# Optimization experiments

Measured on AMD Instinct MI355X. Metric: run time of the kernel, lower is better.

Reference implementation:

```python
import jax, jax.numpy as jnp
import numpy as np

N = 100000      # nodes
E = 1600000     # edges (before self loops)
F_IN = 128      # num_features
HEADS1, CH1 = 8, 8    # conv1: heads=8, out=8, concat -> 64
HEADS2, CH2 = 1, 16   # conv2: heads=1, out=16, concat=False
B = 64          # graphs in batch


def setup_inputs() -> dict:
    key = jax.random.key(0)
    ks = jax.random.split(key, 20)
    s = 0.05
    x = jax.random.normal(ks[0], (N, F_IN), dtype=jnp.float32)
    edge_index = jax.random.randint(ks[1], (2, E), 0, N, dtype=jnp.int64)
    batch = jnp.sort(jax.random.randint(ks[2], (N,), 0, B, dtype=jnp.int64))
    d = {
        'x': x, 'edge_index': edge_index, 'batch': batch,
        # conv1 params (GATv2: lin_l / lin_r with bias, att vector, output bias)
        'Wl1': jax.random.normal(ks[3], (F_IN, HEADS1 * CH1)) * s,
        'bl1': jnp.zeros((HEADS1 * CH1,), jnp.float32),
        'Wr1': jax.random.normal(ks[4], (F_IN, HEADS1 * CH1)) * s,
        'br1': jnp.zeros((HEADS1 * CH1,), jnp.float32),
        'att1': jax.random.normal(ks[5], (HEADS1, CH1)) * s,
        'bias1': jnp.zeros((HEADS1 * CH1,), jnp.float32),
        # conv2 params
        'Wl2': jax.random.normal(ks[6], (HEADS1 * CH1, HEADS2 * CH2)) * s,
        'bl2': jnp.zeros((HEADS2 * CH2,), jnp.float32),
        'Wr2': jax.random.normal(ks[7], (HEADS1 * CH1, HEADS2 * CH2)) * s,
        'br2': jnp.zeros((HEADS2 * CH2,), jnp.float32),
        'att2': jax.random.normal(ks[8], (HEADS2, CH2)) * s,
        'bias2': jnp.zeros((CH2,), jnp.float32),
        # classifier 16 -> 1
        'Wc': jax.random.normal(ks[9], (CH2, 1)) * s,
        'bc': jnp.zeros((1,), jnp.float32),
    }
    return d


def gatv2_layer(x, src, dst, Wl, bl, Wr, br, att, bias, heads, ch, concat):
    n = x.shape[0]
    xl = (x @ Wl + bl).reshape(n, heads, ch)   # source transform (messages)
    xr = (x @ Wr + br).reshape(n, heads, ch)   # target transform
    m = xl[src] + xr[dst]                      # [E, H, C]
    e = jax.nn.leaky_relu(m, 0.2)
    logits = jnp.einsum('ehc,hc->eh', e, att)  # [E, H]
    # segment softmax over incoming edges per target node
    mx = jax.ops.segment_max(logits, dst, num_segments=n)
    mx = jnp.where(jnp.isfinite(mx), mx, 0.0)
    ex = jnp.exp(logits - mx[dst])
    denom = jax.ops.segment_sum(ex, dst, num_segments=n)
    alpha = ex / (denom[dst] + 1e-16)
    out = jax.ops.segment_sum(alpha[:, :, None] * xl[src], dst, num_segments=n)
    out = out.reshape(n, heads * ch) if concat else out.mean(axis=1)
    return out + bias


def reference(x, edge_index, batch, Wl1, bl1, Wr1, br1, att1, bias1,
              Wl2, bl2, Wr2, br2, att2, bias2, Wc, bc):
    n = x.shape[0]
    loops = jnp.arange(n, dtype=edge_index.dtype)
    src = jnp.concatenate([edge_index[0], loops])   # add self loops (PyG default)
    dst = jnp.concatenate([edge_index[1], loops])

    h = gatv2_layer(x, src, dst, Wl1, bl1, Wr1, br1, att1, bias1, HEADS1, CH1, True)
    h = jax.nn.elu(h)
    h = gatv2_layer(h, src, dst, Wl2, bl2, Wr2, br2, att2, bias2, HEADS2, CH2, False)

    counts = jax.ops.segment_sum(jnp.ones((n,), h.dtype), batch, num_segments=B)
    pooled = jax.ops.segment_sum(h, batch, num_segments=B) / jnp.clip(counts, 1.0)[:, None]
    out = (pooled @ Wc + bc).reshape(-1)            # [B]
    return out, pooled
```

## Files before the change

kernel.cpp:

```cpp
#include <hip/hip_runtime.h>
#include <cstdint>
#include <cstddef>

#define F_IN   128
#define HC1    64
#define CH2_   16
#define NB     64
#define BUKPAD 8192

__global__ void fill_f32(float* __restrict__ p, float v, int n) {
  int i = blockIdx.x * blockDim.x + threadIdx.x;
  int stride = gridDim.x * blockDim.x;
  for (; i < n; i += stride) p[i] = v;
}

__device__ __forceinline__ unsigned short f2bf_rne(float v) {
  unsigned int u = __float_as_uint(v);
  unsigned int r = (u + 0x7FFFu + ((u >> 16) & 1u)) >> 16;
  return (unsigned short)r;
}
__device__ __forceinline__ float bf2f(unsigned short b) {
  return __uint_as_float((unsigned int)b << 16);
}

template<int CTRL>
__device__ __forceinline__ float dpp_add(float v) {
  int j = __builtin_amdgcn_update_dpp(0, __float_as_int(v), CTRL, 0xF, 0xF, true);
  return v + __int_as_float(j);
}
__device__ __forceinline__ float sum16_dpp(float v) {
  v = dpp_add<0xB1>(v);
  v = dpp_add<0x4E>(v);
  v = dpp_add<0x141>(v);
  v = dpp_add<0x140>(v);
  return v;
}

__global__ void gemm_dual_l1(const float* __restrict__ x,
                             const float* __restrict__ Wa, const float* __restrict__ ba,
                             const float* __restrict__ Wb, const float* __restrict__ bb,
                             unsigned short* __restrict__ ya, float* __restrict__ yb, int n) {
  constexpr int K = F_IN, M = HC1, BM = 64, NN = 16;
  __shared__ float xs[BM * K];
  const int t = threadIdx.x;
  const int node0 = blockIdx.x * BM;
  for (int i = t; i < BM * (K / 4); i += 256) {
    int row = i / (K / 4);
    int kk  = (i % (K / 4)) * 4;
    int node = node0 + row;
    float4 v = make_float4(0.f, 0.f, 0.f, 0.f);
    if (node < n) v = *reinterpret_cast<const float4*>(x + (size_t)node * K + kk);
    *reinterpret_cast<float4*>(xs + row * K + kk) = v;
  }
  __syncthreads();
  const int col = t % M;
  const int ng  = t / M;
  float accA[NN], accB[NN];
  const float biasA = ba[col], biasB = bb[col];
#pragma unroll
  for (int i = 0; i < NN; ++i) { accA[i] = biasA; accB[i] = biasB; }
  for (int k = 0; k < K; k += 4) {
    float wa0 = Wa[(k + 0) * M + col], wa1 = Wa[(k + 1) * M + col];
    float wa2 = Wa[(k + 2) * M + col], wa3 = Wa[(k + 3) * M + col];
    float wb0 = Wb[(k + 0) * M + col], wb1 = Wb[(k + 1) * M + col];
    float wb2 = Wb[(k + 2) * M + col], wb3 = Wb[(k + 3) * M + col];
#pragma unroll
    for (int nn = 0; nn < NN; ++nn) {
      float4 xv = *reinterpret_cast<const float4*>(xs + (ng * NN + nn) * K + k);
      accA[nn] += xv.x * wa0 + xv.y * wa1 + xv.z * wa2 + xv.w * wa3;
      accB[nn] += xv.x * wb0 + xv.y * wb1 + xv.z * wb2 + xv.w * wb3;
    }
  }
#pragma unroll
  for (int nn = 0; nn < NN; ++nn) {
    int node = node0 + ng * NN + nn;
    if (node < n) {
      ya[(size_t)node * M + col] = f2bf_rne(accA[nn]);
      yb[(size_t)node * M + col] = accB[nn];
    }
  }
}


__global__ void bucket_scatter(const int* __restrict__ ei, int E, int E2,
                               int* __restrict__ gcnt, int* __restrict__ gbuk) {
  __shared__ int hbase[512];
  __shared__ int hcnt[512];
  const int t = threadIdx.x;
  for (int i = t; i < 512; i += 256) { hbase[i] = 0; hcnt[i] = 0; }
  __syncthreads();
  int srcs[32], dsts[32];
  const int tile0 = blockIdx.x * 8192;
#pragma unroll
  for (int k = 0; k < 32; ++k) {
    int e = tile0 + k * 256 + t;
    int s = -1, d = 0;
    if (e < E2) {
      if (e < E) { s = ei[e]; d = ei[E + e]; } else { s = d = e - E; }
      atomicAdd(&hbase[d >> 8], 1);
    }
    srcs[k] = s; dsts[k] = d;
  }
  __syncthreads();
  for (int i = t; i < 512; i += 256) {
    int c = hbase[i];
    hbase[i] = (c > 0) ? atomicAdd(&gcnt[i], c) : 0;
  }
  __syncthreads();
#pragma unroll
  for (int k = 0; k < 32; ++k) {
    if (srcs[k] >= 0) {
      int d = dsts[k], b = d >> 8;
      int r = atomicAdd(&hcnt[b], 1);
      int pl = hbase[b] + r;
      if (pl < BUKPAD) gbuk[(size_t)b * BUKPAD + pl] = (srcs[k] << 8) | (d & 255);
    }
  }
}

__global__ void bucket_prefix(const int* __restrict__ gcnt, int nbuk,
                              int* __restrict__ gbase, int* __restrict__ row_start, int n) {
  int lane = threadIdx.x;
  int carry = 0;
  for (int basei = 0; basei < nbuk; basei += 64) {
    int i = basei + lane;
    int orig = (i < nbuk) ? gcnt[i] : 0;
    int v = orig;
    for (int off = 1; off < 64; off <<= 1) {
      int u = __shfl_up(v, off);
      if (lane >= off) v += u;
    }
    if (i < nbuk) gbase[i] = carry + v - orig;
    carry += __shfl(v, 63);
  }
  if (lane == 0) row_start[n] = carry;
}

__global__ void bucket_csr(const int* __restrict__ gcnt, const int* __restrict__ gbase,
                           const int* __restrict__ gbuk,
                           int* __restrict__ row_start, int* __restrict__ csr_src, int n) {
  const int b = blockIdx.x;
  const int t = threadIdx.x;
  const int node0 = b << 8;
  const int cntb = min(gcnt[b], BUKPAD);
  const int base = gbase[b];
  const int* buk = gbuk + (size_t)b * BUKPAD;
  __shared__ int h[256];
  __shared__ int off[256];
  h[t] = 0;
  __syncthreads();
  for (int i = t; i < cntb; i += 256) atomicAdd(&h[buk[i] & 255], 1);
  __syncthreads();
  off[t] = h[t];
  __syncthreads();
  for (int o = 1; o < 256; o <<= 1) {
    int u = (t >= o) ? off[t - o] : 0;
    __syncthreads();
    off[t] += u;
    __syncthreads();
  }
  int excl = off[t] - h[t];
  if (node0 + t < n) row_start[node0 + t] = base + excl;
  h[t] = excl;
  __syncthreads();
  for (int i = t; i < cntb; i += 256) {
    int p = buk[i];
    int r = atomicAdd(&h[p & 255], 1);
    csr_src[base + r] = p >> 8;
  }
}

__global__ void fused_layer1(const int* __restrict__ row_start, const int* __restrict__ csr_src,
                             const unsigned short* __restrict__ xl, const float* __restrict__ xr,
                             const float* __restrict__ att, const float* __restrict__ bias,
                             const float* __restrict__ Wl2, const float* __restrict__ bl2,
                             const float* __restrict__ Wr2, const float* __restrict__ br2,
                             float* __restrict__ xl2, float* __restrict__ xr2, int n) {
  __shared__ float Ws2[64 * 32];
  __shared__ float b2s[32];
  const int t = threadIdx.x;
  for (int i = t; i < 64 * 16; i += 256) {
    int l = i >> 4, j = i & 15;
    Ws2[l * 32 + j]      = Wl2[i];
    Ws2[l * 32 + 16 + j] = Wr2[i];
  }
  if (t < 16) { b2s[t] = bl2[t]; b2s[16 + t] = br2[t]; }
  __syncthreads();

  const int node = blockIdx.x * 4 + (t >> 6);
  if (node >= n) return;
  const int lane = t & 63;
  const int g = lane >> 4;
  const int q = lane & 15;
  const float4 attv = *reinterpret_cast<const float4*>(att + q * 4);
  const float4 xrv  = *reinterpret_cast<const float4*>(xr + (size_t)node * 64 + q * 4);
  const unsigned short* xlq = xl + q * 4;
  const int beg = row_start[node];
  const int total = row_start[node + 1] - beg;
  const float NEGB = -3.0e38f;
  float den = 0.0f;
  float4 acc = make_float4(0.f, 0.f, 0.f, 0.f);

  for (int base = 0; base < total; base += 64) {
    int idx = base + lane;
    int sidx = csr_src[beg + (idx < total ? idx : total - 1)];
    const int lim = min(64, total - base);
    for (int c0 = 0; c0 < lim; c0 += 8) {
      int iA = c0 + g, iB = c0 + 4 + g;
      int sA = __shfl(sidx, iA);
      int sB = __shfl(sidx, iB);
      ushort4 uA = *reinterpret_cast<const ushort4*>(xlq + (size_t)sA * 64);
      ushort4 uB = *reinterpret_cast<const ushort4*>(xlq + (size_t)sB * 64);
      float xA0 = bf2f(uA.x), xA1 = bf2f(uA.y), xA2 = bf2f(uA.z), xA3 = bf2f(uA.w);
      float aA0 = xA0 + xrv.x; aA0 = fmaxf(aA0, 0.2f * aA0);
      float aA1 = xA1 + xrv.y; aA1 = fmaxf(aA1, 0.2f * aA1);
      float aA2 = xA2 + xrv.z; aA2 = fmaxf(aA2, 0.2f * aA2);
      float aA3 = xA3 + xrv.w; aA3 = fmaxf(aA3, 0.2f * aA3);
      float pA = aA0 * attv.x + aA1 * attv.y + aA2 * attv.z + aA3 * attv.w;
      float vA = dpp_add<0xB1>(pA);
      float exA = __expf(iA < lim ? vA : NEGB);
      den  += exA;
      acc.x += exA * xA0; acc.y += exA * xA1;
      acc.z += exA * xA2; acc.w += exA * xA3;
      float xB0 = bf2f(uB.x), xB1 = bf2f(uB.y), xB2 = bf2f(uB.z), xB3 = bf2f(uB.w);
      float aB0 = xB0 + xrv.x; aB0 = fmaxf(aB0, 0.2f * aB0);
      float aB1 = xB1 + xrv.y; aB1 = fmaxf(aB1, 0.2f * aB1);
      float aB2 = xB2 + xrv.z; aB2 = fmaxf(aB2, 0.2f * aB2);
      float aB3 = xB3 + xrv.w; aB3 = fmaxf(aB3, 0.2f * aB3);
      float pB = aB0 * attv.x + aB1 * attv.y + aB2 * attv.z + aB3 * attv.w;
      float vB = dpp_add<0xB1>(pB);
      float exB = __expf(iB < lim ? vB : NEGB);
      den  += exB;
      acc.x += exB * xB0; acc.y += exB * xB1;
      acc.z += exB * xB2; acc.w += exB * xB3;
    }
  }
  acc.x += __shfl_xor(acc.x, 16); acc.y += __shfl_xor(acc.y, 16);
  acc.z += __shfl_xor(acc.z, 16); acc.w += __shfl_xor(acc.w, 16);
  acc.x += __shfl_xor(acc.x, 32); acc.y += __shfl_xor(acc.y, 32);
  acc.z += __shfl_xor(acc.z, 32); acc.w += __shfl_xor(acc.w, 32);
  den += __shfl_xor(den, 16);
  den += __shfl_xor(den, 32);
  const float inv = 1.0f / (den + 1e-16f);
  const float4 bi = *reinterpret_cast<const float4*>(bias + q * 4);
  float o0 = acc.x * inv + bi.x; o0 = o0 > 0.f ? o0 : __expf(o0) - 1.0f;
  float o1 = acc.y * inv + bi.y; o1 = o1 > 0.f ? o1 : __expf(o1) - 1.0f;
  float o2 = acc.z * inv + bi.z; o2 = o2 > 0.f ? o2 : __expf(o2) - 1.0f;
  float o3 = acc.w * inv + bi.w; o3 = o3 > 0.f ? o3 : __expf(o3) - 1.0f;

  int srcl = lane >> 2;
  float c0 = __shfl(o0, srcl);
  float c1 = __shfl(o1, srcl);
  float c2 = __shfl(o2, srcl);
  float c3 = __shfl(o3, srcl);
  int r = lane & 3;
  float o = (r == 0) ? c0 : (r == 1) ? c1 : (r == 2) ? c2 : c3;

  const int j    = lane & 31;
  const int half = lane >> 5;
  float part2 = 0.0f;
#pragma unroll 8
  for (int l = 0; l < 32; ++l) {
    int src = half * 32 + l;
    float ov = __shfl(o, src);
    part2 += ov * Ws2[src * 32 + j];
  }
  part2 += __shfl_xor(part2, 32);
  if (lane < 16)      xl2[(size_t)node * 16 + j]        = part2 + b2s[j];
  else if (lane < 32) xr2[(size_t)node * 16 + (j - 16)] = part2 + b2s[j];
}

__global__ void fused_layer2(const int* __restrict__ row_start, const int* __restrict__ csr_src,
                             const float* __restrict__ xl, const float* __restrict__ xr,
                             const float* __restrict__ att, const float* __restrict__ bias,
                             float* __restrict__ out, int n) {
  int node = blockIdx.x * 16 + (threadIdx.x >> 4);
  if (node >= n) return;
  int c = threadIdx.x & 15;
  const float attv = att[c];
  const float xrv  = xr[(size_t)node * 16 + c];
  const int beg = row_start[node], end = row_start[node + 1];
  float den = 0.0f, acc = 0.0f;
  int p = beg;
  for (; p + 4 <= end; p += 4) {
    int s0 = csr_src[p + 0], s1 = csr_src[p + 1];
    int s2 = csr_src[p + 2], s3 = csr_src[p + 3];
    float x0 = xl[(size_t)s0 * 16 + c];
    float x1 = xl[(size_t)s1 * 16 + c];
    float x2 = xl[(size_t)s2 * 16 + c];
    float x3 = xl[(size_t)s3 * 16 + c];
    float a0 = x0 + xrv; a0 = a0 > 0.f ? a0 : 0.2f * a0;
    float a1 = x1 + xrv; a1 = a1 > 0.f ? a1 : 0.2f * a1;
    float a2 = x2 + xrv; a2 = a2 > 0.f ? a2 : 0.2f * a2;
    float a3 = x3 + xrv; a3 = a3 > 0.f ? a3 : 0.2f * a3;
    float e0 = __expf(sum16_dpp(a0 * attv));
    float e1 = __expf(sum16_dpp(a1 * attv));
    float e2 = __expf(sum16_dpp(a2 * attv));
    float e3 = __expf(sum16_dpp(a3 * attv));
    den += (e0 + e1) + (e2 + e3);
    acc += (e0 * x0 + e1 * x1) + (e2 * x2 + e3 * x3);
  }
  for (; p < end; ++p) {
    int s = csr_src[p];
    float xv = xl[(size_t)s * 16 + c];
    float a = xv + xrv; a = a > 0.f ? a : 0.2f * a;
    float ex = __expf(sum16_dpp(a * attv));
    den += ex;
    acc += ex * xv;
  }
  out[(size_t)node * 16 + c] = acc / (den + 1e-16f) + bias[c];
}


__global__ void pool_kernel(const float* __restrict__ h2, const int* __restrict__ batch,
                            float* __restrict__ sums, float* __restrict__ cnts, int n) {
  __shared__ float ls[NB * CH2_];
  __shared__ float lc[NB];
  for (int i = threadIdx.x; i < NB * CH2_; i += blockDim.x) ls[i] = 0.0f;
  for (int i = threadIdx.x; i < NB; i += blockDim.x) lc[i] = 0.0f;
  __syncthreads();
  int total = n * 16;
  int stride = gridDim.x * blockDim.x;
  for (int i = blockIdx.x * blockDim.x + threadIdx.x; i < total; i += stride) {
    int node = i >> 4, c = i & 15;
    int b = batch[node];
    atomicAdd(&ls[b * 16 + c], h2[i]);
    if (c == 0) atomicAdd(&lc[b], 1.0f);
  }
  __syncthreads();
  for (int i = threadIdx.x; i < NB * CH2_; i += blockDim.x)
    if (ls[i] != 0.0f) atomicAdd(&sums[i], ls[i]);
  for (int i = threadIdx.x; i < NB; i += blockDim.x)
    if (lc[i] != 0.0f) atomicAdd(&cnts[i], lc[i]);
}

__global__ void classifier(const float* __restrict__ sums, const float* __restrict__ cnts,
                           const float* __restrict__ Wc, const float* __restrict__ bc,
                           float* __restrict__ out) {
  int b = threadIdx.x;
  if (b >= NB) return;
  float cnt = cnts[b];
  cnt = cnt > 1.0f ? cnt : 1.0f;
  float acc = 0.0f;
  for (int c = 0; c < 16; ++c) {
    float p = sums[b * 16 + c] / cnt;
    out[NB + b * 16 + c] = p;
    acc += p * Wc[c];
  }
  out[b] = acc + bc[0];
}

extern "C" void kernel_launch(void* const* d_in, const int* in_sizes, int n_in,
                              void* d_out, int out_size, void* d_ws, size_t ws_size,
                              hipStream_t stream) {
  const float* x     = (const float*)d_in[0];
  const int*   ei    = (const int*)d_in[1];
  const int*   batch = (const int*)d_in[2];
  const float* Wl1   = (const float*)d_in[3];
  const float* bl1   = (const float*)d_in[4];
  const float* Wr1   = (const float*)d_in[5];
  const float* br1   = (const float*)d_in[6];
  const float* att1  = (const float*)d_in[7];
  const float* bias1 = (const float*)d_in[8];
  const float* Wl2   = (const float*)d_in[9];
  const float* bl2   = (const float*)d_in[10];
  const float* Wr2   = (const float*)d_in[11];
  const float* br2   = (const float*)d_in[12];
  const float* att2  = (const float*)d_in[13];
  const float* bias2 = (const float*)d_in[14];
  const float* Wc    = (const float*)d_in[15];
  const float* bc    = (const float*)d_in[16];
  float* out = (float*)d_out;

  const int N  = in_sizes[0] / F_IN;
  const int E  = in_sizes[1] / 2;
  const int E2 = E + N;
  const int nbuk = (N + 255) >> 8;

  float* ws   = (float*)d_ws;
  unsigned short* xl1 = (unsigned short*)ws;
  float* xr1  = (float*)(xl1 + (size_t)N * 64);
  float* xl2  = xr1 + (size_t)N * 64;
  float* xr2  = xl2 + (size_t)N * 16;
  float* h2   = xr2 + (size_t)N * 16;
  int* irow   = (int*)(h2 + (size_t)N * 16);
  int* icsr   = irow + (N + 1);
  int* gcnt   = icsr + E2;
  int* gbase  = gcnt + 512;
  int* gbuk   = gbase + 513 + 2;
  float* sums = (float*)(gbuk + (size_t)nbuk * BUKPAD);
  float* cnts = sums + NB * CH2_;

  fill_f32<<<1, 256, 0, stream>>>((float*)gcnt, 0.0f, 512);
  bucket_scatter<<<(E2 + 8191) / 8192, 256, 0, stream>>>(ei, E, E2, gcnt, gbuk);
  bucket_prefix<<<1, 64, 0, stream>>>(gcnt, nbuk, gbase, irow, N);
  bucket_csr<<<nbuk, 256, 0, stream>>>(gcnt, gbase, gbuk, irow, icsr, N);

  gemm_dual_l1<<<(N + 63) / 64, 256, 0, stream>>>(
      x, Wl1, bl1, Wr1, br1, xl1, xr1, N);

  fused_layer1<<<(N + 3) / 4, 256, 0, stream>>>(
      irow, icsr, xl1, xr1, att1, bias1, Wl2, bl2, Wr2, br2, xl2, xr2, N);

  fused_layer2<<<(N + 15) / 16, 256, 0, stream>>>(irow, icsr, xl2, xr2, att2, bias2, h2, N);

  fill_f32<<<1, 256, 0, stream>>>(sums, 0.0f, NB * CH2_ + NB);
  pool_kernel<<<256, 256, 0, stream>>>(h2, batch, sums, cnts, N);
  classifier<<<1, 64, 0, stream>>>(sums, cnts, Wc, bc, out);
}
```

Before: 264.9 us.

## Replace scalar layer-1 dual GEMM with bf16 MFMA using hi/lo split

The FP32 FMA GEMM that computes both lin_l and lin_r for layer 1 is replaced with an MFMA 16x16x32 bf16 kernel. Each x value is split into hi and lo bf16 parts to keep close to fp32 accuracy. A new pre-kernel packs Wl1 and Wr1 into bf16 fragment layout, and results are staged through LDS for coalesced stores. This moves the GEMM from vector ALUs to matrix cores, at the cost of one extra launch, weights rounded to bf16, and larger LDS use that may lower occupancy.

```diff
diff --git a/kernel.cpp b/kernel.cpp
--- a/kernel.cpp
+++ b/kernel.cpp
@@ -7,6 +7,9 @@
 #define CH2_   16
 #define NB     64
 #define BUKPAD 8192
+
+typedef __attribute__((ext_vector_type(8))) short bf16x8;
+typedef __attribute__((ext_vector_type(4))) float f32x4;
 
 __global__ void fill_f32(float* __restrict__ p, float v, int n) {
   int i = blockIdx.x * blockDim.x + threadIdx.x;
@@ -36,48 +39,90 @@
   return v;
 }
 
-__global__ void gemm_dual_l1(const float* __restrict__ x,
-                             const float* __restrict__ Wa, const float* __restrict__ ba,
-                             const float* __restrict__ Wb, const float* __restrict__ bb,
-                             unsigned short* __restrict__ ya, float* __restrict__ yb, int n) {
-  constexpr int K = F_IN, M = HC1, BM = 64, NN = 16;
-  __shared__ float xs[BM * K];
+
+__global__ void build_wfrag(const float* __restrict__ Wl, const float* __restrict__ Wr,
+                            unsigned short* __restrict__ wfrag) {
+  int idx = blockIdx.x * 256 + threadIdx.x;
+  if (idx >= 16384) return;
+  int e    = idx & 7;
+  int lane = (idx >> 3) & 63;
+  int tile = (idx >> 9) & 7;
+  int ks   = idx >> 12;
+  int k    = ks * 32 + (lane >> 4) * 8 + e;
+  int col  = tile * 16 + (lane & 15);
+  float v = (col < 64) ? Wl[k * 64 + col] : Wr[k * 64 + (col - 64)];
+  wfrag[idx] = f2bf_rne(v);
+}
+
+__global__ __launch_bounds__(256) void gemm_mfma_l1(
+    const float* __restrict__ x, const unsigned short* __restrict__ wfrag,
+    const float* __restrict__ bl, const float* __restrict__ br,
+    unsigned short* __restrict__ ya, float* __restrict__ yb, int n) {
+  constexpr int RP = 136;
+  __shared__ __align__(16) char smem[34816 + 32768];
+  unsigned short* axhi = (unsigned short*)smem;
+  unsigned short* axlo = (unsigned short*)(smem + 17408);
+  unsigned short* wf   = (unsigned short*)(smem + 34816);
+  float* outs = (float*)smem;
+
   const int t = threadIdx.x;
-  const int node0 = blockIdx.x * BM;
-  for (int i = t; i < BM * (K / 4); i += 256) {
-    int row = i / (K / 4);
-    int kk  = (i % (K / 4)) * 4;
+  const int node0 = blockIdx.x * 64;
+
+  for (int i = t; i < 2048; i += 256)
+    reinterpret_cast<int4*>(wf)[i] = reinterpret_cast<const int4*>(wfrag)[i];
+  for (int i = t; i < 64 * 32; i += 256) {
+    int row = i >> 5, kk = (i & 31) * 4;
     int node = node0 + row;
     float4 v = make_float4(0.f, 0.f, 0.f, 0.f);
-    if (node < n) v = *reinterpret_cast<const float4*>(x + (size_t)node * K + kk);
-    *reinterpret_cast<float4*>(xs + row * K + kk) = v;
-  }
-  __syncthreads();
-  const int col = t % M;
-  const int ng  = t / M;
-  float accA[NN], accB[NN];
-  const float biasA = ba[col], biasB = bb[col];
-#pragma unroll
-  for (int i = 0; i < NN; ++i) { accA[i] = biasA; accB[i] = biasB; }
-  for (int k = 0; k < K; k += 4) {
-    float wa0 = Wa[(k + 0) * M + col], wa1 = Wa[(k + 1) * M + col];
-    float wa2 = Wa[(k + 2) * M + col], wa3 = Wa[(k + 3) * M + col];
-    float wb0 = Wb[(k + 0) * M + col], wb1 = Wb[(k + 1) * M + col];
-    float wb2 = Wb[(k + 2) * M + col], wb3 = Wb[(k + 3) * M + col];
-#pragma unroll
-    for (int nn = 0; nn < NN; ++nn) {
-      float4 xv = *reinterpret_cast<const float4*>(xs + (ng * NN + nn) * K + k);
-      accA[nn] += xv.x * wa0 + xv.y * wa1 + xv.z * wa2 + xv.w * wa3;
-      accB[nn] += xv.x * wb0 + xv.y * wb1 + xv.z * wb2 + xv.w * wb3;
-    }
-  }
-#pragma unroll
-  for (int nn = 0; nn < NN; ++nn) {
-    int node = node0 + ng * NN + nn;
-    if (node < n) {
-      ya[(size_t)node * M + col] = f2bf_rne(accA[nn]);
-      yb[(size_t)node * M + col] = accB[nn];
-    }
+    if (node < n) v = *reinterpret_cast<const float4*>(x + (size_t)node * 128 + kk);
+    ushort4 hi, lo;
+    hi.x = f2bf_rne(v.x); lo.x = f2bf_rne(v.x - bf2f(hi.x));
+    hi.y = f2bf_rne(v.y); lo.y = f2bf_rne(v.y - bf2f(hi.y));
+    hi.z = f2bf_rne(v.z); lo.z = f2bf_rne(v.z - bf2f(hi.z));
+    hi.w = f2bf_rne(v.w); lo.w = f2bf_rne(v.w - bf2f(hi.w));
+    *reinterpret_cast<ushort4*>(axhi + row * RP + kk) = hi;
+    *reinterpret_cast<ushort4*>(axlo + row * RP + kk) = lo;
+  }
+  __syncthreads();
+
+  const int wv   = t >> 6;
+  const int lane = t & 63;
+  const int mrow = lane & 15;
+  const int kg   = lane >> 4;
+  f32x4 acc[8];
+#pragma unroll
+  for (int i = 0; i < 8; ++i) acc[i] = (f32x4){0.f, 0.f, 0.f, 0.f};
+  const int abase = (wv * 16 + mrow) * RP;
+#pragma unroll
+  for (int ks = 0; ks < 4; ++ks) {
+    int aoff = abase + ks * 32 + kg * 8;
+    bf16x8 ahi = *reinterpret_cast<const bf16x8*>(axhi + aoff);
+    bf16x8 alo = *reinterpret_cast<const bf16x8*>(axlo + aoff);
+#pragma unroll
+    for (int tl = 0; tl < 8; ++tl) {
+      bf16x8 b = *reinterpret_cast<const bf16x8*>(wf + ((ks * 8 + tl) * 64 + lane) * 8);
+      acc[tl] = __builtin_amdgcn_mfma_f32_16x16x32_bf16(alo, b, acc[tl], 0, 0, 0);
+      acc[tl] = __builtin_amdgcn_mfma_f32_16x16x32_bf16(ahi, b, acc[tl], 0, 0, 0);
+    }
+  }
+  __syncthreads();
+#pragma unroll
+  for (int tl = 0; tl < 8; ++tl)
+#pragma unroll
+    for (int r = 0; r < 4; ++r) {
+      int row = wv * 16 + kg * 4 + r;
+      outs[row * 128 + tl * 16 + mrow] = acc[tl][r];
+    }
+  __syncthreads();
+  for (int i = t; i < 64 * 64; i += 256) {
+    int row = i >> 6, col = i & 63;
+    int node = node0 + row;
+    if (node < n) ya[(size_t)node * 64 + col] = f2bf_rne(outs[row * 128 + col] + bl[col]);
+  }
+  for (int i = t; i < 64 * 64; i += 256) {
+    int row = i >> 6, col = i & 63;
+    int node = node0 + row;
+    if (node < n) yb[(size_t)node * 64 + col] = outs[row * 128 + 64 + col] + br[col];
   }
 }
 
@@ -388,7 +433,9 @@
   int* gcnt   = icsr + E2;
   int* gbase  = gcnt + 512;
   int* gbuk   = gbase + 513 + 2;
-  float* sums = (float*)(gbuk + (size_t)nbuk * BUKPAD);
+  unsigned short* wfrag =
+      (unsigned short*)(((uintptr_t)(gbuk + (size_t)nbuk * BUKPAD) + 15) & ~(uintptr_t)15);
+  float* sums = (float*)(wfrag + 16384);
   float* cnts = sums + NB * CH2_;
 
   fill_f32<<<1, 256, 0, stream>>>((float*)gcnt, 0.0f, 512);
@@ -396,8 +443,8 @@
   bucket_prefix<<<1, 64, 0, stream>>>(gcnt, nbuk, gbase, irow, N);
   bucket_csr<<<nbuk, 256, 0, stream>>>(gcnt, gbase, gbuk, irow, icsr, N);
 
-  gemm_dual_l1<<<(N + 63) / 64, 256, 0, stream>>>(
-      x, Wl1, bl1, Wr1, br1, xl1, xr1, N);
+  build_wfrag<<<64, 256, 0, stream>>>(Wl1, Wr1, wfrag);
+  gemm_mfma_l1<<<(N + 63) / 64, 256, 0, stream>>>(x, wfrag, bl1, br1, xl1, xr1, N);
 
   fused_layer1<<<(N + 3) / 4, 256, 0, stream>>>(
       irow, icsr, xl1, xr1, att1, bias1, Wl2, bl2, Wr2, br2, xl2, xr2, N);
```

After: 234.5 us. 1.13x faster.
